# Kernel optimization log

Hardware: AMD Instinct MI355X
Metric: run time of the kernel (lower is better)

Reference implementation:

```python
import jax, jax.numpy as jnp
import numpy as np

N = 2097152  # batch of FP32 bit-vectors

# --- logic gates on {0,1} float spikes (faithful to FullAdder/NOT/OR/AND/MUX neurons) ---

def _xor(a, b):
    return a + b - 2.0 * a * b

def _mux(sel, a, b):  # MUXGate(sel, a, b) = a if sel else b
    return sel * a + (1.0 - sel) * b

def _full_adder(a, b, c):  # returns (sum, carry)
    x = _xor(a, b)
    return _xor(x, c), a * b + c * x

def _shift_hi(v, n):  # output[i] = v[i-n], zeros shifted in at the MSB side
    pad = jnp.zeros(v.shape[:-1] + (n,), v.dtype)
    return jnp.concatenate([pad, v[..., :-n]], axis=-1)


def setup_inputs() -> dict:
    key = jax.random.key(0)
    k1, k2 = jax.random.split(key)
    # random 0/1 bit patterns (binary spikes), FP32 bit layout [sign | 8 exp | 23 mant]
    x = jnp.round(jax.random.uniform(k1, (N, 32), dtype=jnp.float32))
    k = jnp.round(jax.random.uniform(k2, (N, 32), dtype=jnp.float32))
    return {"x": x, "k": k}


def reference(x, k):
    batch = x.shape[:-1]
    zeros = jnp.zeros(batch + (1,), x.dtype)
    ones = jnp.ones(batch + (1,), x.dtype)

    s_x, e_x, m_x = x[..., 0:1], x[..., 1:9], x[..., 9:32]
    s_k, e_k, m_k = k[..., 0:1], k[..., 1:9], k[..., 9:32]

    # shift = e_k - 127 via two's complement: e_k + NOT(127) + 1 (little-endian ripple)
    e_k_le = jnp.flip(e_k, -1)
    const_127_le = jnp.concatenate([ones] * 7 + [zeros], axis=-1)
    not_127_le = 1.0 - const_127_le  # NOTGate chain
    shift_bits = []
    borrow = ones
    for i in range(8):
        s, borrow = _full_adder(e_k_le[..., i:i + 1], not_127_le[..., i:i + 1], borrow)
        shift_bits.append(s)
    shift = jnp.concatenate(shift_bits, -1)  # little-endian unbiased exponent

    # barrel shifter on [implicit-1, top 7 mantissa bits] (big-endian), sel = NOT(shift bit)
    val = jnp.concatenate([ones, m_k[..., 0:7]], axis=-1)
    s_bar0 = 1.0 - shift[..., 0:1]
    s_bar1 = 1.0 - shift[..., 1:2]
    s_bar2 = 1.0 - shift[..., 2:3]
    l0 = _mux(s_bar0, _shift_hi(val, 1), val)
    l1 = _mux(s_bar1, _shift_hi(l0, 2), l0)
    l2 = _mux(s_bar2, _shift_hi(l1, 4), l1)
    k_abs_le = jnp.flip(l2, -1)

    # negate |k| (two's complement): NOT(k_abs) + 1
    not_k = 1.0 - k_abs_le
    neg_bits = []
    carry = ones
    for i in range(8):
        s, carry = _full_adder(not_k[..., i:i + 1], zeros, carry)
        neg_bits.append(s)
    neg_k = jnp.concatenate(neg_bits, -1)

    # pick signed k, add to exponent of x (ripple adder, little-endian)
    k_final = _mux(s_k, neg_k, k_abs_le)
    e_x_le = jnp.flip(e_x, -1)
    e_new_bits = []
    carry = zeros
    for i in range(8):
        s, carry = _full_adder(e_x_le[..., i:i + 1], k_final[..., i:i + 1], carry)
        e_new_bits.append(s)
    e_new = jnp.flip(jnp.concatenate(e_new_bits, -1), -1)

    # k == 0 detection: NOT(OR of exp bits) AND NOT(OR of mantissa bits)
    # OR-reduce of binary bits == 1 - prod(1 - bit); NOT gives prod(1 - bit)
    k_e_zero_n = jnp.prod(1.0 - e_k, axis=-1, keepdims=True)
    k_m_zero_n = jnp.prod(1.0 - m_k, axis=-1, keepdims=True)
    k_is_zero = k_e_zero_n * k_m_zero_n  # ANDGate

    result_scaled = jnp.concatenate([s_x, e_new, m_x], axis=-1)
    # final 32-bit MUX: pass x through unchanged when k == 0
    return _mux(k_is_zero, x, result_scaled)
```

## Files before the change

kernel.cpp:

```cpp
#include <hip/hip_runtime.h>


__device__ __forceinline__ unsigned rev8(unsigned v) {
    return __builtin_bitreverse32(v) >> 24;
}

__global__ __launch_bounds__(256) void spike_scale_kernel(
        const float4* __restrict__ x4,
        const float4* __restrict__ k4,
        float4* __restrict__ o4,
        int nvec) {
    int idx = blockIdx.x * 256 + threadIdx.x;
    if (idx >= nvec) return;

    float4 vx = x4[idx];
    float4 vk = k4[idx];

    unsigned g    = (unsigned)(idx & 7);
    unsigned base = g * 4u;

    unsigned nibx = (unsigned)(vx.x != 0.0f)
                  | ((unsigned)(vx.y != 0.0f) << 1)
                  | ((unsigned)(vx.z != 0.0f) << 2)
                  | ((unsigned)(vx.w != 0.0f) << 3);
    unsigned nibk = (unsigned)(vk.x != 0.0f)
                  | ((unsigned)(vk.y != 0.0f) << 1)
                  | ((unsigned)(vk.z != 0.0f) << 2)
                  | ((unsigned)(vk.w != 0.0f) << 3);

    unsigned long long w = ((unsigned long long)nibx << base)
                         | ((unsigned long long)nibk << (32u + base));
    w |= __shfl_xor(w, 1);
    w |= __shfl_xor(w, 2);
    w |= __shfl_xor(w, 4);

    unsigned xw = (unsigned)w;
    unsigned kw = (unsigned)(w >> 32);

    unsigned ek   = rev8((kw >> 1) & 0xFFu);
    unsigned val  = 0x80u | (__builtin_bitreverse32((kw >> 9) & 0x7Fu) >> 25);
    unsigned s    = (ek - 127u) & 7u;
    unsigned kabs = val >> (7u - s);
    unsigned kfin = (kw & 1u) ? ((0u - kabs) & 0xFFu) : kabs;

    unsigned ex   = rev8((xw >> 1) & 0xFFu);
    unsigned enew = (ex + kfin) & 0xFFu;

    unsigned scaled = (xw & 1u) | (rev8(enew) << 1) | (xw & 0xFFFFFE00u);
    unsigned res    = ((kw & ~1u) == 0u) ? xw : scaled;

    float4 out;
    out.x = (float)((res >> (base + 0u)) & 1u);
    out.y = (float)((res >> (base + 1u)) & 1u);
    out.z = (float)((res >> (base + 2u)) & 1u);
    out.w = (float)((res >> (base + 3u)) & 1u);
    o4[idx] = out;
}

extern "C" void kernel_launch(void* const* d_in, const int* in_sizes, int n_in,
                              void* d_out, int out_size, void* d_ws, size_t ws_size,
                              hipStream_t stream) {
    const float4* x4 = (const float4*)d_in[0];
    const float4* k4 = (const float4*)d_in[1];
    float4* o4 = (float4*)d_out;

    int n_elems = in_sizes[0];
    int nvec    = n_elems / 4;
    int blocks  = (nvec + 255) / 256;

    spike_scale_kernel<<<blocks, 256, 0, stream>>>(x4, k4, o4, nvec);
}
```

Measured before the change: 572.8 us.

## Process one full 32-bit row per thread instead of shuffling nibbles

Each thread now loads a whole row (8 uint4 each for x and k), packs the bits by reading bit 23 of each float's raw integer (1.0f has it set, 0.0f does not), and writes all 8 output float4s. This drops the three cross-lane 64-bit shuffles and the float compares. The cost is that each thread's accesses are strided 128 bytes apart across lanes, so loads and stores are no longer coalesced per instruction, and there are 8x fewer threads with more registers each.

```diff
diff --git a/kernel.cpp b/kernel.cpp
--- a/kernel.cpp
+++ b/kernel.cpp
@@ -5,37 +5,37 @@
     return __builtin_bitreverse32(v) >> 24;
 }
 
-__global__ __launch_bounds__(256) void spike_scale_kernel(
-        const float4* __restrict__ x4,
-        const float4* __restrict__ k4,
+__global__ __launch_bounds__(256) void spike_scale_row_kernel(
+        const uint4* __restrict__ x4,
+        const uint4* __restrict__ k4,
         float4* __restrict__ o4,
-        int nvec) {
-    int idx = blockIdx.x * 256 + threadIdx.x;
-    if (idx >= nvec) return;
+        int nrows) {
+    int row = blockIdx.x * 256 + threadIdx.x;
+    if (row >= nrows) return;
 
-    float4 vx = x4[idx];
-    float4 vk = k4[idx];
+    const uint4* xr = x4 + (size_t)row * 8;
+    const uint4* kr = k4 + (size_t)row * 8;
 
-    unsigned g    = (unsigned)(idx & 7);
-    unsigned base = g * 4u;
+    uint4 vx[8], vk[8];
+#pragma unroll
+    for (int j = 0; j < 8; ++j) vx[j] = xr[j];
+#pragma unroll
+    for (int j = 0; j < 8; ++j) vk[j] = kr[j];
 
-    unsigned nibx = (unsigned)(vx.x != 0.0f)
-                  | ((unsigned)(vx.y != 0.0f) << 1)
-                  | ((unsigned)(vx.z != 0.0f) << 2)
-                  | ((unsigned)(vx.w != 0.0f) << 3);
-    unsigned nibk = (unsigned)(vk.x != 0.0f)
-                  | ((unsigned)(vk.y != 0.0f) << 1)
-                  | ((unsigned)(vk.z != 0.0f) << 2)
-                  | ((unsigned)(vk.w != 0.0f) << 3);
-
-    unsigned long long w = ((unsigned long long)nibx << base)
-                         | ((unsigned long long)nibk << (32u + base));
-    w |= __shfl_xor(w, 1);
-    w |= __shfl_xor(w, 2);
-    w |= __shfl_xor(w, 4);
-
-    unsigned xw = (unsigned)w;
-    unsigned kw = (unsigned)(w >> 32);
+    unsigned xw = 0u, kw = 0u;
+#pragma unroll
+    for (int j = 0; j < 8; ++j) {
+        unsigned nx = ((vx[j].x >> 23) & 1u)
+                    | (((vx[j].y >> 23) & 1u) << 1)
+                    | (((vx[j].z >> 23) & 1u) << 2)
+                    | (((vx[j].w >> 23) & 1u) << 3);
+        unsigned nk = ((vk[j].x >> 23) & 1u)
+                    | (((vk[j].y >> 23) & 1u) << 1)
+                    | (((vk[j].z >> 23) & 1u) << 2)
+                    | (((vk[j].w >> 23) & 1u) << 3);
+        xw |= nx << (4 * j);
+        kw |= nk << (4 * j);
+    }
 
     unsigned ek   = rev8((kw >> 1) & 0xFFu);
     unsigned val  = 0x80u | (__builtin_bitreverse32((kw >> 9) & 0x7Fu) >> 25);
@@ -49,24 +49,28 @@
     unsigned scaled = (xw & 1u) | (rev8(enew) << 1) | (xw & 0xFFFFFE00u);
     unsigned res    = ((kw & ~1u) == 0u) ? xw : scaled;
 
-    float4 out;
-    out.x = (float)((res >> (base + 0u)) & 1u);
-    out.y = (float)((res >> (base + 1u)) & 1u);
-    out.z = (float)((res >> (base + 2u)) & 1u);
-    out.w = (float)((res >> (base + 3u)) & 1u);
-    o4[idx] = out;
+    float4* orow = o4 + (size_t)row * 8;
+#pragma unroll
+    for (int j = 0; j < 8; ++j) {
+        float4 o;
+        o.x = ((res >> (4 * j + 0)) & 1u) ? 1.0f : 0.0f;
+        o.y = ((res >> (4 * j + 1)) & 1u) ? 1.0f : 0.0f;
+        o.z = ((res >> (4 * j + 2)) & 1u) ? 1.0f : 0.0f;
+        o.w = ((res >> (4 * j + 3)) & 1u) ? 1.0f : 0.0f;
+        orow[j] = o;
+    }
 }
 
 extern "C" void kernel_launch(void* const* d_in, const int* in_sizes, int n_in,
                               void* d_out, int out_size, void* d_ws, size_t ws_size,
                               hipStream_t stream) {
-    const float4* x4 = (const float4*)d_in[0];
-    const float4* k4 = (const float4*)d_in[1];
+    const uint4* x4 = (const uint4*)d_in[0];
+    const uint4* k4 = (const uint4*)d_in[1];
     float4* o4 = (float4*)d_out;
 
     int n_elems = in_sizes[0];
-    int nvec    = n_elems / 4;
-    int blocks  = (nvec + 255) / 256;
+    int nrows   = n_elems / 32;
+    int blocks  = (nrows + 255) / 256;
 
-    spike_scale_kernel<<<blocks, 256, 0, stream>>>(x4, k4, o4, nvec);
+    spike_scale_row_kernel<<<blocks, 256, 0, stream>>>(x4, k4, o4, nrows);
 }
```

Measured after the change: 639.6 us. 1.12x slower.
